# Kernel tuning notes

Hardware: AMD Instinct MI355X
Metric: run time of the kernel (lower is better)

Reference implementation:

```python
import jax, jax.numpy as jnp
import numpy as np

B, T, D, L, H = 4096, 512, 16, 6, 1  # batch, seq_len, input_size, num_layers, hidden_size


def setup_inputs() -> dict:
    key = jax.random.key(0)
    ks = jax.random.split(key, 6)
    s = 1.0  # PyTorch init: uniform(-1/sqrt(H), 1/sqrt(H)) with H=1
    x = jax.random.normal(ks[0], (B, T, D), dtype=jnp.float32)
    w_ih0 = jax.random.uniform(ks[1], (4 * H, D), jnp.float32, -s, s)
    w_ih_rest = jax.random.uniform(ks[2], (L - 1, 4 * H, H), jnp.float32, -s, s)
    w_hh = jax.random.uniform(ks[3], (L, 4 * H, H), jnp.float32, -s, s)
    b_ih = jax.random.uniform(ks[4], (L, 4 * H), jnp.float32, -s, s)
    b_hh = jax.random.uniform(ks[5], (L, 4 * H), jnp.float32, -s, s)
    return {"x": x, "w_ih0": w_ih0, "w_ih_rest": w_ih_rest,
            "w_hh": w_hh, "b_ih": b_ih, "b_hh": b_hh}


def _lstm_layer(xproj, w_hh_l):
    """xproj: [T, B, 4H] input projections (biases already added). Returns h seq [T, B, H]."""
    bsz = xproj.shape[1]
    h0 = jnp.zeros((bsz, H), xproj.dtype)
    c0 = jnp.zeros((bsz, H), xproj.dtype)

    def step(carry, g_x):
        h, c = carry
        g = g_x + h @ w_hh_l.T          # [B, 4H], PyTorch gate order i,f,g,o
        i, f, gg, o = jnp.split(g, 4, axis=-1)
        c = jax.nn.sigmoid(f) * c + jax.nn.sigmoid(i) * jnp.tanh(gg)
        h = jax.nn.sigmoid(o) * jnp.tanh(c)
        return (h, c), h

    _, hs = jax.lax.scan(step, (h0, c0), xproj)
    return hs


def reference(x, w_ih0, w_ih_rest, w_hh, b_ih, b_hh):
    # eval-mode 6-layer stacked LSTM (dropout disabled), batch_first input
    inp = jnp.swapaxes(x, 0, 1)  # [T, B, D]
    for l in range(L):
        w_ih = w_ih0 if l == 0 else w_ih_rest[l - 1]
        xproj = inp @ w_ih.T + (b_ih[l] + b_hh[l])  # [T, B, 4H]
        inp = _lstm_layer(xproj, w_hh[l])           # [T, B, H]
    # y[:, -1, 0]: last timestep, hidden channel 0 of top layer
    return inp[-1, :, 0]
```

## Files before the change

### kernel.cpp

```cpp
#include <hip/hip_runtime.h>

constexpr int Tn = 512;
constexpr int Bn = 4096;
constexpr int CH = 32;
constexpr int NCH = Tn / CH;

constexpr float NL2E = -1.44269504088896340736f;
constexpr float P2L2E = 2.88539008177792681472f;

#if defined(__has_builtin)
#if __has_builtin(__builtin_amdgcn_exp2f)
#define EXP2F(x) __builtin_amdgcn_exp2f(x)
#else
#define EXP2F(x) exp2f(x)
#endif
#else
#define EXP2F(x) exp2f(x)
#endif

__device__ __forceinline__ float dpp_shr1(float v) {
  return __int_as_float(__builtin_amdgcn_update_dpp(
      __float_as_int(v), __float_as_int(v), 0x111, 0xf, 0xf, false));
}

template <bool GATED>
__device__ __forceinline__ void tick(float& h, float& c, const float4 pre,
                                     const float4 wih, const float4 whh,
                                     unsigned tau, unsigned lg) {
  const float h_in = dpp_shr1(h);
  const float tg = fmaf(h, whh.z, pre.z);
  const float ti = fmaf(h, whh.x, pre.x);
  const float tf = fmaf(h, whh.y, pre.y);
  const float to = fmaf(h, whh.w, pre.w);
  const float ag = fmaf(h_in, wih.z, tg);
  const float ai = fmaf(h_in, wih.x, ti);
  const float af = fmaf(h_in, wih.y, tf);
  const float ao = fmaf(h_in, wih.w, to);
  const float Eg = EXP2F(ag);
  const float Ei = EXP2F(ai);
  const float Ef = EXP2F(af);
  const float Eo = EXP2F(ao);
  const float v = 1.0f + Eg;
  const float u = 1.0f + Ei;
  const float Q = 1.0f + Ef;
  const float P = u * v;
  const float QP = Q * P;
  const float R = __builtin_amdgcn_rcpf(QP);
  const float sig_o = __builtin_amdgcn_rcpf(1.0f + Eo);
  const float ws = fmaf(P2L2E, Eg, -P2L2E);
  const float num = fmaf(c, P, ws * Q);
  const float cn = num * R;
  const float Ec = EXP2F(cn);
  const float rt = __builtin_amdgcn_rcpf(1.0f + Ec);
  const float th = fmaf(-2.0f, rt, 1.0f);
  const float hn = sig_o * th;
  if (GATED) {
    const bool act = (tau - lg) < (unsigned)Tn;
    c = act ? cn : c;
    h = act ? hn : h;
  } else {
    c = cn;
    h = hn;
  }
}

__global__ __launch_bounds__(64, 1) void lstm_fused_kernel(
    const float* __restrict__ x, const float* __restrict__ w_ih0,
    const float* __restrict__ w_ih_rest, const float* __restrict__ w_hh,
    const float* __restrict__ b_ih, const float* __restrict__ b_hh,
    float* __restrict__ out) {
  __shared__ __align__(16) float4 bufA[CH * 8];
  __shared__ __align__(16) float4 bufB[CH * 8];
  __shared__ __align__(16) float4 biasRep[32 * 8];

  const int ln = threadIdx.x;
  const int bW = blockIdx.x * 8;
  const int ge = ln >> 3;
  const unsigned lg = ln & 7;
  const bool is0l = (lg == 0);
  const int ep = ln & 7;
  const int t8p = ln >> 3;

  const int l = (lg < 6) ? (int)lg : 5;
  float4 whh = make_float4(NL2E * w_hh[l * 4 + 0], NL2E * w_hh[l * 4 + 1],
                           P2L2E * w_hh[l * 4 + 2], NL2E * w_hh[l * 4 + 3]);
  float4 wih = make_float4(0.f, 0.f, 0.f, 0.f);
  float4 bz = make_float4(0.f, 0.f, 0.f, 0.f);
  if (lg >= 1 && lg < 6) {
    wih = make_float4(NL2E * w_ih_rest[(l - 1) * 4 + 0],
                      NL2E * w_ih_rest[(l - 1) * 4 + 1],
                      P2L2E * w_ih_rest[(l - 1) * 4 + 2],
                      NL2E * w_ih_rest[(l - 1) * 4 + 3]);
    bz = make_float4(NL2E * (b_ih[lg * 4 + 0] + b_hh[lg * 4 + 0]),
                     NL2E * (b_ih[lg * 4 + 1] + b_hh[lg * 4 + 1]),
                     P2L2E * (b_ih[lg * 4 + 2] + b_hh[lg * 4 + 2]),
                     NL2E * (b_ih[lg * 4 + 3] + b_hh[lg * 4 + 3]));
  }
  if (lg >= 6) whh = make_float4(0.f, 0.f, 0.f, 0.f);

#pragma unroll
  for (int rep = 0; rep < 4; ++rep) biasRep[rep * 64 + ln] = bz;

  const char* rbA = is0l ? (const char*)(bufA + ge) : (const char*)(biasRep + (int)lg);
  const char* rbB = is0l ? (const char*)(bufB + ge) : (const char*)(biasRep + (int)lg);

  float w[4][16], pb[4];
  {
    const float sc[4] = {NL2E, NL2E, P2L2E, NL2E};
#pragma unroll
    for (int g = 0; g < 4; ++g) {
      pb[g] = sc[g] * (b_ih[g] + b_hh[g]);
#pragma unroll
      for (int d = 0; d < 16; ++d) w[g][d] = sc[g] * w_ih0[g * 16 + d];
    }
  }

  const float4* x4 = (const float4*)x;
  float4 xs[16];
  float h = 0.f, c = 0.f;
  float4 pA[8], pB[8];

  auto LOADC = [&](int ci) {
    const size_t base = ((size_t)(bW + ep) * Tn + (size_t)ci * CH + t8p) * 4;
#pragma unroll
    for (int k = 0; k < 4; ++k)
#pragma unroll
      for (int i = 0; i < 4; ++i) xs[k * 4 + i] = x4[base + (size_t)k * 32 + i];
  };
  auto PROJq = [&](float4* dst, int k) {
    float s0 = pb[0], s1 = pb[1], s2 = pb[2], s3 = pb[3];
#pragma unroll
    for (int i = 0; i < 4; ++i) {
      const float4 a = xs[k * 4 + i];
      s0 = fmaf(a.x, w[0][i * 4 + 0], s0); s0 = fmaf(a.y, w[0][i * 4 + 1], s0);
      s0 = fmaf(a.z, w[0][i * 4 + 2], s0); s0 = fmaf(a.w, w[0][i * 4 + 3], s0);
      s1 = fmaf(a.x, w[1][i * 4 + 0], s1); s1 = fmaf(a.y, w[1][i * 4 + 1], s1);
      s1 = fmaf(a.z, w[1][i * 4 + 2], s1); s1 = fmaf(a.w, w[1][i * 4 + 3], s1);
      s2 = fmaf(a.x, w[2][i * 4 + 0], s2); s2 = fmaf(a.y, w[2][i * 4 + 1], s2);
      s2 = fmaf(a.z, w[2][i * 4 + 2], s2); s2 = fmaf(a.w, w[2][i * 4 + 3], s2);
      s3 = fmaf(a.x, w[3][i * 4 + 0], s3); s3 = fmaf(a.y, w[3][i * 4 + 1], s3);
      s3 = fmaf(a.z, w[3][i * 4 + 2], s3); s3 = fmaf(a.w, w[3][i * 4 + 3], s3);
    }
    dst[ln + 64 * k] = make_float4(s0, s1, s2, s3);
  };
  auto RD = [&](float4* p, const char* b, int jb) {
#pragma unroll
    for (int k = 0; k < 8; ++k)
      p[k] = *(const float4*)(b + (size_t)((jb * 8 + k) * 128));
  };
  auto T = [&](float4* p) {
#pragma unroll
    for (int k = 0; k < 8; ++k) tick<false>(h, c, p[k], wih, whh, 0u, 0u);
  };
  auto Tg = [&](float4* p, unsigned tau0) {
#pragma unroll
    for (int k = 0; k < 8; ++k)
      tick<true>(h, c, p[k], wih, whh, tau0 + (unsigned)k, lg);
  };

  LOADC(0);
#pragma unroll
  for (int k = 0; k < 4; ++k) PROJq(bufA, k);
  LOADC(1);
  RD(pA, rbA, 0);

  RD(pB, rbA, 1);  Tg(pA, 0u);
  RD(pA, rbA, 2);  T(pB);
  PROJq(bufB, 0);  PROJq(bufB, 1);
  RD(pB, rbA, 3);  T(pA);
  PROJq(bufB, 2);  PROJq(bufB, 3);
  RD(pA, rbB, 0);  T(pB);
  LOADC(2);

#pragma unroll 1
  for (int j = 1; j < NCH; ++j) {
    const char* rc = (j & 1) ? rbB : rbA;
    const char* rn = (j & 1) ? rbA : rbB;
    float4* bn = (j & 1) ? bufA : bufB;
    RD(pB, rc, 1);  T(pA);
    RD(pA, rc, 2);  T(pB);
    if (j < NCH - 1) { PROJq(bn, 0); PROJq(bn, 1); }
    RD(pB, rc, 3);  T(pA);
    if (j < NCH - 1) { PROJq(bn, 2); PROJq(bn, 3); }
    RD(pA, (j < NCH - 1) ? rn : rc, 0);  T(pB);
    if (j < NCH - 2) LOADC(j + 2);
  }

#pragma unroll
  for (unsigned k = 0; k < 5; ++k)
    tick<true>(h, c, bz, wih, whh, 512u + k, lg);

  if (lg == 5) out[bW + ge] = h;
}

extern "C" void kernel_launch(void* const* d_in, const int* in_sizes, int n_in,
                              void* d_out, int out_size, void* d_ws, size_t ws_size,
                              hipStream_t stream) {
  (void)in_sizes; (void)n_in; (void)out_size; (void)d_ws; (void)ws_size;
  const float* x         = (const float*)d_in[0];
  const float* w_ih0     = (const float*)d_in[1];
  const float* w_ih_rest = (const float*)d_in[2];
  const float* w_hh      = (const float*)d_in[3];
  const float* b_ih      = (const float*)d_in[4];
  const float* b_hh      = (const float*)d_in[5];
  float* out = (float*)d_out;

  lstm_fused_kernel<<<Bn / 8, 64, 0, stream>>>(x, w_ih0, w_ih_rest, w_hh,
                                               b_ih, b_hh, out);
}
```

Baseline: 54.70 us.

## Interleave input projection and loads with recurrent ticks, merge rcp in tanh

Spreads the layer-0 input projection FMAs and the next-chunk global loads across the serial LSTM tick sequence instead of issuing them in bursts between tick groups, so the latency-bound recurrence can hide that independent work. It rewrites the projection with 4-wide vector FMAs and merges the sigmoid(o) and tanh(c) reciprocals into a single rcp, clamping the exponent to avoid overflow. The risks are extra register pressure and runtime MODE branches inside the unrolled loop, plus a small change in numerical behaviour.

```diff
diff --git a/kernel.cpp b/kernel.cpp
--- a/kernel.cpp
+++ b/kernel.cpp
@@ -7,6 +7,8 @@
 
 constexpr float NL2E = -1.44269504088896340736f;
 constexpr float P2L2E = 2.88539008177792681472f;
+
+typedef float f4 __attribute__((ext_vector_type(4)));
 
 #if defined(__has_builtin)
 #if __has_builtin(__builtin_amdgcn_exp2f)
@@ -46,14 +48,14 @@
   const float P = u * v;
   const float QP = Q * P;
   const float R = __builtin_amdgcn_rcpf(QP);
-  const float sig_o = __builtin_amdgcn_rcpf(1.0f + Eo);
   const float ws = fmaf(P2L2E, Eg, -P2L2E);
   const float num = fmaf(c, P, ws * Q);
   const float cn = num * R;
-  const float Ec = EXP2F(cn);
-  const float rt = __builtin_amdgcn_rcpf(1.0f + Ec);
-  const float th = fmaf(-2.0f, rt, 1.0f);
-  const float hn = sig_o * th;
+  const float Ec = EXP2F(fminf(cn, 80.0f));
+  const float so = 1.0f + Eo;
+  const float t2 = 1.0f + Ec;
+  const float R2 = __builtin_amdgcn_rcpf(so * t2);
+  const float hn = (Ec - 1.0f) * R2;
   if (GATED) {
     const bool act = (tau - lg) < (unsigned)Tn;
     c = act ? cn : c;
@@ -104,15 +106,15 @@
   const char* rbA = is0l ? (const char*)(bufA + ge) : (const char*)(biasRep + (int)lg);
   const char* rbB = is0l ? (const char*)(bufB + ge) : (const char*)(biasRep + (int)lg);
 
-  float w[4][16], pb[4];
+  f4 wv[16], pbv;
   {
     const float sc[4] = {NL2E, NL2E, P2L2E, NL2E};
 #pragma unroll
-    for (int g = 0; g < 4; ++g) {
-      pb[g] = sc[g] * (b_ih[g] + b_hh[g]);
-#pragma unroll
-      for (int d = 0; d < 16; ++d) w[g][d] = sc[g] * w_ih0[g * 16 + d];
-    }
+    for (int d = 0; d < 16; ++d)
+      wv[d] = (f4){sc[0] * w_ih0[0 * 16 + d], sc[1] * w_ih0[1 * 16 + d],
+                   sc[2] * w_ih0[2 * 16 + d], sc[3] * w_ih0[3 * 16 + d]};
+    pbv = (f4){sc[0] * (b_ih[0] + b_hh[0]), sc[1] * (b_ih[1] + b_hh[1]),
+               sc[2] * (b_ih[2] + b_hh[2]), sc[3] * (b_ih[3] + b_hh[3])};
   }
 
   const float4* x4 = (const float4*)x;
@@ -127,35 +129,54 @@
 #pragma unroll
       for (int i = 0; i < 4; ++i) xs[k * 4 + i] = x4[base + (size_t)k * 32 + i];
   };
-  auto PROJq = [&](float4* dst, int k) {
-    float s0 = pb[0], s1 = pb[1], s2 = pb[2], s3 = pb[3];
-#pragma unroll
-    for (int i = 0; i < 4; ++i) {
-      const float4 a = xs[k * 4 + i];
-      s0 = fmaf(a.x, w[0][i * 4 + 0], s0); s0 = fmaf(a.y, w[0][i * 4 + 1], s0);
-      s0 = fmaf(a.z, w[0][i * 4 + 2], s0); s0 = fmaf(a.w, w[0][i * 4 + 3], s0);
-      s1 = fmaf(a.x, w[1][i * 4 + 0], s1); s1 = fmaf(a.y, w[1][i * 4 + 1], s1);
-      s1 = fmaf(a.z, w[1][i * 4 + 2], s1); s1 = fmaf(a.w, w[1][i * 4 + 3], s1);
-      s2 = fmaf(a.x, w[2][i * 4 + 0], s2); s2 = fmaf(a.y, w[2][i * 4 + 1], s2);
-      s2 = fmaf(a.z, w[2][i * 4 + 2], s2); s2 = fmaf(a.w, w[2][i * 4 + 3], s2);
-      s3 = fmaf(a.x, w[3][i * 4 + 0], s3); s3 = fmaf(a.y, w[3][i * 4 + 1], s3);
-      s3 = fmaf(a.z, w[3][i * 4 + 2], s3); s3 = fmaf(a.w, w[3][i * 4 + 3], s3);
-    }
-    dst[ln + 64 * k] = make_float4(s0, s1, s2, s3);
+  auto PROJsub = [&](f4& sv, int qk, int i) {
+    const float4 a = xs[qk * 4 + i];
+    sv = __builtin_elementwise_fma((f4){a.x, a.x, a.x, a.x}, wv[i * 4 + 0], sv);
+    sv = __builtin_elementwise_fma((f4){a.y, a.y, a.y, a.y}, wv[i * 4 + 1], sv);
+    sv = __builtin_elementwise_fma((f4){a.z, a.z, a.z, a.z}, wv[i * 4 + 2], sv);
+    sv = __builtin_elementwise_fma((f4){a.w, a.w, a.w, a.w}, wv[i * 4 + 3], sv);
+  };
+  auto PROJq = [&](float4* dst, int qk) {
+    f4 sv = pbv;
+#pragma unroll
+    for (int i = 0; i < 4; ++i) PROJsub(sv, qk, i);
+    *(f4*)&dst[ln + 64 * qk] = sv;
   };
   auto RD = [&](float4* p, const char* b, int jb) {
 #pragma unroll
     for (int k = 0; k < 8; ++k)
       p[k] = *(const float4*)(b + (size_t)((jb * 8 + k) * 128));
   };
-  auto T = [&](float4* p) {
-#pragma unroll
-    for (int k = 0; k < 8; ++k) tick<false>(h, c, p[k], wih, whh, 0u, 0u);
-  };
-  auto Tg = [&](float4* p, unsigned tau0) {
-#pragma unroll
-    for (int k = 0; k < 8; ++k)
+  auto T8W = [&](float4* p, int MODE, float4* dst, int qk, int ci) {
+    f4 sv = pbv;
+    size_t lbase = 0;
+    if (MODE == 2)
+      lbase = ((size_t)(bW + ep) * Tn + (size_t)ci * CH + t8p) * 4;
+#pragma unroll
+    for (int k = 0; k < 8; ++k) {
+      tick<false>(h, c, p[k], wih, whh, 0u, 0u);
+      if (MODE >= 1 && k < 4) {
+        PROJsub(sv, qk, k);
+        if (k == 3) *(f4*)&dst[ln + 64 * qk] = sv;
+      }
+      if (MODE == 2 && k >= 4) {
+        const int m = k - 4;
+#pragma unroll
+        for (int i = 0; i < 4; ++i)
+          xs[m * 4 + i] = x4[lbase + (size_t)m * 32 + i];
+      }
+    }
+  };
+  auto T8Wg = [&](float4* p, float4* dst, int qk, unsigned tau0) {
+    f4 sv = pbv;
+#pragma unroll
+    for (int k = 0; k < 8; ++k) {
       tick<true>(h, c, p[k], wih, whh, tau0 + (unsigned)k, lg);
+      if (k < 4) {
+        PROJsub(sv, qk, k);
+        if (k == 3) *(f4*)&dst[ln + 64 * qk] = sv;
+      }
+    }
   };
 
   LOADC(0);
@@ -164,26 +185,23 @@
   LOADC(1);
   RD(pA, rbA, 0);
 
-  RD(pB, rbA, 1);  Tg(pA, 0u);
-  RD(pA, rbA, 2);  T(pB);
-  PROJq(bufB, 0);  PROJq(bufB, 1);
-  RD(pB, rbA, 3);  T(pA);
-  PROJq(bufB, 2);  PROJq(bufB, 3);
-  RD(pA, rbB, 0);  T(pB);
-  LOADC(2);
+  RD(pB, rbA, 1);  T8Wg(pA, bufB, 0, 0u);
+  RD(pA, rbA, 2);  T8W(pB, 1, bufB, 1, 0);
+  RD(pB, rbA, 3);  T8W(pA, 1, bufB, 2, 0);
+  RD(pA, rbB, 0);  T8W(pB, 2, bufB, 3, 2);
 
 #pragma unroll 1
   for (int j = 1; j < NCH; ++j) {
     const char* rc = (j & 1) ? rbB : rbA;
     const char* rn = (j & 1) ? rbA : rbB;
     float4* bn = (j & 1) ? bufA : bufB;
-    RD(pB, rc, 1);  T(pA);
-    RD(pA, rc, 2);  T(pB);
-    if (j < NCH - 1) { PROJq(bn, 0); PROJq(bn, 1); }
-    RD(pB, rc, 3);  T(pA);
-    if (j < NCH - 1) { PROJq(bn, 2); PROJq(bn, 3); }
-    RD(pA, (j < NCH - 1) ? rn : rc, 0);  T(pB);
-    if (j < NCH - 2) LOADC(j + 2);
+    const int m1 = (j < NCH - 1) ? 1 : 0;
+    RD(pB, rc, 1);  T8W(pA, m1, bn, 0, 0);
+    RD(pA, rc, 2);  T8W(pB, m1, bn, 1, 0);
+    RD(pB, rc, 3);  T8W(pA, m1, bn, 2, 0);
+    const int m3 = (j < NCH - 2) ? 2 : m1;
+    RD(pA, (j < NCH - 1) ? rn : rc, 0);
+    T8W(pB, m3, bn, 3, j + 2);
   }
 
 #pragma unroll
```

Result: slower. 69.37 us (+26.8%).

## Split each LSTM layer's gates across lane pairs, halving per-lane serial work

Applied to the files above, without the earlier changes.

Each layer now uses two lanes instead of one. One lane computes the i and g gates, the other f and o, and DPP swaps exchange partial products and reciprocals between the pair. The wavefront holds 4 batch elements instead of 8, so the grid doubles, and the shared projection buffer becomes a single float2 double buffer with bias prefilled. The goal is to shorten the serial per-tick dependency chain of the wavefront-pipelined recurrence, at the cost of twice as many wavefronts and extra DPP cross-lane latency on each step.

```diff
diff --git a/kernel.cpp b/kernel.cpp
--- a/kernel.cpp
+++ b/kernel.cpp
@@ -18,44 +18,50 @@
 #define EXP2F(x) exp2f(x)
 #endif
 
-__device__ __forceinline__ float dpp_shr1(float v) {
+__device__ __forceinline__ float dpp_pair_even(float v) {
   return __int_as_float(__builtin_amdgcn_update_dpp(
-      __float_as_int(v), __float_as_int(v), 0x111, 0xf, 0xf, false));
+      __float_as_int(v), __float_as_int(v), 0xA0, 0xf, 0xf, false));
+}
+__device__ __forceinline__ float dpp_pair_odd(float v) {
+  return __int_as_float(__builtin_amdgcn_update_dpp(
+      __float_as_int(v), __float_as_int(v), 0xF5, 0xf, 0xf, false));
+}
+__device__ __forceinline__ float dpp_shr2(float v) {
+  return __int_as_float(__builtin_amdgcn_update_dpp(
+      __float_as_int(v), __float_as_int(v), 0x112, 0xf, 0xf, false));
 }
 
 template <bool GATED>
-__device__ __forceinline__ void tick(float& h, float& c, const float4 pre,
-                                     const float4 wih, const float4 whh,
-                                     unsigned tau, unsigned lg) {
-  const float h_in = dpp_shr1(h);
-  const float tg = fmaf(h, whh.z, pre.z);
-  const float ti = fmaf(h, whh.x, pre.x);
-  const float tf = fmaf(h, whh.y, pre.y);
-  const float to = fmaf(h, whh.w, pre.w);
-  const float ag = fmaf(h_in, wih.z, tg);
-  const float ai = fmaf(h_in, wih.x, ti);
-  const float af = fmaf(h_in, wih.y, tf);
-  const float ao = fmaf(h_in, wih.w, to);
-  const float Eg = EXP2F(ag);
-  const float Ei = EXP2F(ai);
-  const float Ef = EXP2F(af);
-  const float Eo = EXP2F(ao);
-  const float v = 1.0f + Eg;
-  const float u = 1.0f + Ei;
-  const float Q = 1.0f + Ef;
-  const float P = u * v;
-  const float QP = Q * P;
-  const float R = __builtin_amdgcn_rcpf(QP);
-  const float sig_o = __builtin_amdgcn_rcpf(1.0f + Eo);
-  const float ws = fmaf(P2L2E, Eg, -P2L2E);
-  const float num = fmaf(c, P, ws * Q);
-  const float cn = num * R;
+__device__ __forceinline__ void tick(float& h, float& c, const float2 pre,
+                                     const float2 wih, const float2 whh,
+                                     bool podd, unsigned tau, unsigned l) {
+  const float hb = dpp_pair_even(h);
+  const float h_in = dpp_shr2(hb);
+  const float tA = fmaf(hb, whh.x, pre.x);
+  const float tB = fmaf(hb, whh.y, pre.y);
+  const float aA = fmaf(h_in, wih.x, tA);
+  const float aB = fmaf(h_in, wih.y, tB);
+  const float EA = EXP2F(aA);
+  const float EB = EXP2F(aB);
+  const float sA = 1.0f + EA;
+  const float sB = 1.0f + EB;
+  const float m = sA * sB;
+  const float Qx = dpp_pair_odd(sA);
+  const float qm = Qx * m;
+  const float rin = podd ? sB : qm;
+  const float RC = __builtin_amdgcn_rcpf(rin);
+  const float sgo = dpp_pair_odd(RC);
+  const float ws = fmaf(P2L2E, EB, -P2L2E);
+  const float wsQ = ws * Qx;
+  const float num = fmaf(c, m, wsQ);
+  const float cn = num * RC;
   const float Ec = EXP2F(cn);
-  const float rt = __builtin_amdgcn_rcpf(1.0f + Ec);
+  const float t2 = 1.0f + Ec;
+  const float rt = __builtin_amdgcn_rcpf(t2);
   const float th = fmaf(-2.0f, rt, 1.0f);
-  const float hn = sig_o * th;
+  const float hn = sgo * th;
   if (GATED) {
-    const bool act = (tau - lg) < (unsigned)Tn;
+    const bool act = (tau - l) < (unsigned)Tn;
     c = act ? cn : c;
     h = act ? hn : h;
   } else {
@@ -69,40 +75,37 @@
     const float* __restrict__ w_ih_rest, const float* __restrict__ w_hh,
     const float* __restrict__ b_ih, const float* __restrict__ b_hh,
     float* __restrict__ out) {
-  __shared__ __align__(16) float4 bufA[CH * 8];
-  __shared__ __align__(16) float4 bufB[CH * 8];
-  __shared__ __align__(16) float4 biasRep[32 * 8];
+  __shared__ __align__(16) float2 buf[2][CH][64];
 
   const int ln = threadIdx.x;
-  const int bW = blockIdx.x * 8;
-  const int ge = ln >> 3;
-  const unsigned lg = ln & 7;
-  const bool is0l = (lg == 0);
-  const int ep = ln & 7;
-  const int t8p = ln >> 3;
-
-  const int l = (lg < 6) ? (int)lg : 5;
-  float4 whh = make_float4(NL2E * w_hh[l * 4 + 0], NL2E * w_hh[l * 4 + 1],
-                           P2L2E * w_hh[l * 4 + 2], NL2E * w_hh[l * 4 + 3]);
-  float4 wih = make_float4(0.f, 0.f, 0.f, 0.f);
-  float4 bz = make_float4(0.f, 0.f, 0.f, 0.f);
-  if (lg >= 1 && lg < 6) {
-    wih = make_float4(NL2E * w_ih_rest[(l - 1) * 4 + 0],
-                      NL2E * w_ih_rest[(l - 1) * 4 + 1],
-                      P2L2E * w_ih_rest[(l - 1) * 4 + 2],
-                      NL2E * w_ih_rest[(l - 1) * 4 + 3]);
-    bz = make_float4(NL2E * (b_ih[lg * 4 + 0] + b_hh[lg * 4 + 0]),
-                     NL2E * (b_ih[lg * 4 + 1] + b_hh[lg * 4 + 1]),
-                     P2L2E * (b_ih[lg * 4 + 2] + b_hh[lg * 4 + 2]),
-                     NL2E * (b_ih[lg * 4 + 3] + b_hh[lg * 4 + 3]));
-  }
-  if (lg >= 6) whh = make_float4(0.f, 0.f, 0.f, 0.f);
-
-#pragma unroll
-  for (int rep = 0; rep < 4; ++rep) biasRep[rep * 64 + ln] = bz;
-
-  const char* rbA = is0l ? (const char*)(bufA + ge) : (const char*)(biasRep + (int)lg);
-  const char* rbB = is0l ? (const char*)(bufB + ge) : (const char*)(biasRep + (int)lg);
+  const int bW = blockIdx.x * 4;
+  const int eT = ln >> 4;
+  const int rlane = ln & 15;
+  const unsigned l = (unsigned)(rlane >> 1);
+  const bool podd = (rlane & 1) != 0;
+  const int eP = ln & 3;
+  const int tq = ln >> 2;
+
+  const int lc = (l < 6) ? (int)l : 5;
+  const int gA = podd ? 1 : 0;
+  const int gB = podd ? 3 : 2;
+  const float scB = podd ? NL2E : P2L2E;
+  float2 whh = make_float2(NL2E * w_hh[lc * 4 + gA], scB * w_hh[lc * 4 + gB]);
+  float2 wih = make_float2(0.f, 0.f);
+  float2 bz = make_float2(0.f, 0.f);
+  if (l >= 1 && l < 6) {
+    wih = make_float2(NL2E * w_ih_rest[(lc - 1) * 4 + gA],
+                      scB * w_ih_rest[(lc - 1) * 4 + gB]);
+    bz = make_float2(NL2E * (b_ih[l * 4 + gA] + b_hh[l * 4 + gA]),
+                     scB * (b_ih[l * 4 + gB] + b_hh[l * 4 + gB]));
+  }
+  if (l >= 6) whh = make_float2(0.f, 0.f);
+
+#pragma unroll 1
+  for (int r = 0; r < CH; ++r) {
+    buf[0][r][ln] = bz;
+    buf[1][r][ln] = bz;
+  }
 
   float w[4][16], pb[4];
   {
@@ -116,22 +119,21 @@
   }
 
   const float4* x4 = (const float4*)x;
-  float4 xs[16];
+  float4 xs[8];
   float h = 0.f, c = 0.f;
-  float4 pA[8], pB[8];
-
-  auto LOADC = [&](int ci) {
-    const size_t base = ((size_t)(bW + ep) * Tn + (size_t)ci * CH + t8p) * 4;
-#pragma unroll
-    for (int k = 0; k < 4; ++k)
-#pragma unroll
-      for (int i = 0; i < 4; ++i) xs[k * 4 + i] = x4[base + (size_t)k * 32 + i];
-  };
-  auto PROJq = [&](float4* dst, int k) {
+  float2 pA[8], pB[8];
+
+  auto LOADH = [&](int ci, int hf) {
+    const size_t base =
+        ((size_t)(bW + eP) * Tn + (size_t)(ci * CH + tq + 16 * hf)) * 4;
+#pragma unroll
+    for (int i = 0; i < 4; ++i) xs[hf * 4 + i] = x4[base + i];
+  };
+  auto PROJH = [&](int bi, int hf) {
     float s0 = pb[0], s1 = pb[1], s2 = pb[2], s3 = pb[3];
 #pragma unroll
     for (int i = 0; i < 4; ++i) {
-      const float4 a = xs[k * 4 + i];
+      const float4 a = xs[hf * 4 + i];
       s0 = fmaf(a.x, w[0][i * 4 + 0], s0); s0 = fmaf(a.y, w[0][i * 4 + 1], s0);
       s0 = fmaf(a.z, w[0][i * 4 + 2], s0); s0 = fmaf(a.w, w[0][i * 4 + 3], s0);
       s1 = fmaf(a.x, w[1][i * 4 + 0], s1); s1 = fmaf(a.y, w[1][i * 4 + 1], s1);
@@ -141,56 +143,51 @@
       s3 = fmaf(a.x, w[3][i * 4 + 0], s3); s3 = fmaf(a.y, w[3][i * 4 + 1], s3);
       s3 = fmaf(a.z, w[3][i * 4 + 2], s3); s3 = fmaf(a.w, w[3][i * 4 + 3], s3);
     }
-    dst[ln + 64 * k] = make_float4(s0, s1, s2, s3);
-  };
-  auto RD = [&](float4* p, const char* b, int jb) {
+    const int r = tq + 16 * hf;
+    buf[bi][r][eP * 16 + 0] = make_float2(s0, s2);
+    buf[bi][r][eP * 16 + 1] = make_float2(s1, s3);
+  };
+  auto RD = [&](float2* p, int bi, int jb) {
+#pragma unroll
+    for (int k = 0; k < 8; ++k) p[k] = buf[bi][jb * 8 + k][ln];
+  };
+  auto T8 = [&](float2* p) {
 #pragma unroll
     for (int k = 0; k < 8; ++k)
-      p[k] = *(const float4*)(b + (size_t)((jb * 8 + k) * 128));
-  };
-  auto T = [&](float4* p) {
-#pragma unroll
-    for (int k = 0; k < 8; ++k) tick<false>(h, c, p[k], wih, whh, 0u, 0u);
-  };
-  auto Tg = [&](float4* p, unsigned tau0) {
+      tick<false>(h, c, p[k], wih, whh, podd, 0u, 0u);
+  };
+  auto T8g = [&](float2* p, unsigned tau0) {
 #pragma unroll
     for (int k = 0; k < 8; ++k)
-      tick<true>(h, c, p[k], wih, whh, tau0 + (unsigned)k, lg);
-  };
-
-  LOADC(0);
-#pragma unroll
-  for (int k = 0; k < 4; ++k) PROJq(bufA, k);
-  LOADC(1);
-  RD(pA, rbA, 0);
-
-  RD(pB, rbA, 1);  Tg(pA, 0u);
-  RD(pA, rbA, 2);  T(pB);
-  PROJq(bufB, 0);  PROJq(bufB, 1);
-  RD(pB, rbA, 3);  T(pA);
-  PROJq(bufB, 2);  PROJq(bufB, 3);
-  RD(pA, rbB, 0);  T(pB);
-  LOADC(2);
+      tick<true>(h, c, p[k], wih, whh, podd, tau0 + (unsigned)k, l);
+  };
+
+  LOADH(0, 0); LOADH(0, 1);
+  PROJH(0, 0); PROJH(0, 1);
+  LOADH(1, 0); LOADH(1, 1);
+  RD(pA, 0, 0);
+
+  RD(pB, 0, 1);  T8g(pA, 0u);  PROJH(1, 0);
+  RD(pA, 0, 2);  T8(pB);       PROJH(1, 1);
+  RD(pB, 0, 3);  T8(pA);       LOADH(2, 0);
+  RD(pA, 1, 0);  T8(pB);       LOADH(2, 1);
 
 #pragma unroll 1
   for (int j = 1; j < NCH; ++j) {
-    const char* rc = (j & 1) ? rbB : rbA;
-    const char* rn = (j & 1) ? rbA : rbB;
-    float4* bn = (j & 1) ? bufA : bufB;
-    RD(pB, rc, 1);  T(pA);
-    RD(pA, rc, 2);  T(pB);
-    if (j < NCH - 1) { PROJq(bn, 0); PROJq(bn, 1); }
-    RD(pB, rc, 3);  T(pA);
-    if (j < NCH - 1) { PROJq(bn, 2); PROJq(bn, 3); }
-    RD(pA, (j < NCH - 1) ? rn : rc, 0);  T(pB);
-    if (j < NCH - 2) LOADC(j + 2);
+    const int cur = j & 1, nxt = cur ^ 1;
+    const bool mp = (j < NCH - 1);
+    const bool ml = (j < NCH - 2);
+    RD(pB, cur, 1);  T8(pA);  if (mp) PROJH(nxt, 0);
+    RD(pA, cur, 2);  T8(pB);  if (mp) PROJH(nxt, 1);
+    RD(pB, cur, 3);  T8(pA);  if (ml) LOADH(j + 2, 0);
+    RD(pA, mp ? nxt : cur, 0);  T8(pB);  if (ml) LOADH(j + 2, 1);
   }
 
 #pragma unroll
   for (unsigned k = 0; k < 5; ++k)
-    tick<true>(h, c, bz, wih, whh, 512u + k, lg);
-
-  if (lg == 5) out[bW + ge] = h;
+    tick<true>(h, c, pA[k], wih, whh, podd, 512u + k, l);
+
+  if (rlane == 10) out[bW + eT] = h;
 }
 
 extern "C" void kernel_launch(void* const* d_in, const int* in_sizes, int n_in,
@@ -205,6 +202,6 @@
   const float* b_hh      = (const float*)d_in[5];
   float* out = (float*)d_out;
 
-  lstm_fused_kernel<<<Bn / 8, 64, 0, stream>>>(x, w_ih0, w_ih_rest, w_hh,
+  lstm_fused_kernel<<<Bn / 4, 64, 0, stream>>>(x, w_ih0, w_ih_rest, w_hh,
                                                b_ih, b_hh, out);
 }
```

After: 45.90 us. 1.19x faster.
